# Kernel optimization log

Measured on AMD Instinct MI355X. Metric: run time of the kernel, lower is better.

## Reference

```python
import jax, jax.numpy as jnp
import numpy as np

DN = ('NCHW', 'OIHW', 'NCHW')

def conv1x1(x, w):
    return jax.lax.conv_general_dilated(x, w, (1, 1), 'VALID', dimension_numbers=DN)

def dwconv3(x, w):
    # depthwise 3x3, padding 1; w: (C,1,3,3)
    return jax.lax.conv_general_dilated(x, w, (1, 1), ((1, 1), (1, 1)),
                                        dimension_numbers=DN,
                                        feature_group_count=w.shape[0])

def ln_c(x, w, b, eps=1e-5):
    # Restormer-style LayerNorm over channel dim per spatial location (biased var)
    mu = x.mean(axis=1, keepdims=True)
    var = x.var(axis=1, keepdims=True)
    return (x - mu) / jnp.sqrt(var + eps) * w[None, :, None, None] + b[None, :, None, None]

def gelu(x):
    return jax.nn.gelu(x, approximate=False)

DIM = 128
NUM_HEADS = 2
B, H, W = 4, 192, 192
RED = 16

def setup_inputs() -> dict:
    key = jax.random.key(0)
    ks = jax.random.split(key, 20)
    s = 0.02
    d = DIM
    inp = {
        'x': jax.random.normal(ks[0], (B, d, H, W), jnp.float32),
        'ln_in_w': jnp.ones((d,), jnp.float32),
        'ln_in_b': jnp.zeros((d,), jnp.float32),
        'wq_pw': jax.random.normal(ks[1], (d, d, 1, 1), jnp.float32) * s,
        'wq_dw': jax.random.normal(ks[2], (d, 1, 3, 3), jnp.float32) * s,
        'wk_pw': jax.random.normal(ks[3], (d, d, 1, 1), jnp.float32) * s,
        'wk_dw': jax.random.normal(ks[4], (d, 1, 3, 3), jnp.float32) * s,
        'wv_pw': jax.random.normal(ks[5], (d, d, 1, 1), jnp.float32) * s,
        'wv_dw': jax.random.normal(ks[6], (d, 1, 3, 3), jnp.float32) * s,
        'scale': jnp.ones((NUM_HEADS, 1, 1), jnp.float32),
        'ln_out_w': jnp.ones((d,), jnp.float32),
        'ln_out_b': jnp.zeros((d,), jnp.float32),
        'f1_pw': jax.random.normal(ks[7], (d, d, 1, 1), jnp.float32) * s,
        'f1_dw': jax.random.normal(ks[8], (d, 1, 3, 3), jnp.float32) * s,
        'f2_pw': jax.random.normal(ks[9], (d, d, 1, 1), jnp.float32) * s,
        'f2_dw': jax.random.normal(ks[10], (d, 1, 3, 3), jnp.float32) * s,
        'f_out': jax.random.normal(ks[11], (d, 2 * d, 1, 1), jnp.float32) * s,
        'g_w1': jax.random.normal(ks[12], (d // RED, d), jnp.float32) * s,
        'g_b1': jnp.zeros((d // RED,), jnp.float32),
        'g_w2': jax.random.normal(ks[13], (d, d // RED), jnp.float32) * s,
        'g_b2': jnp.zeros((d,), jnp.float32),
    }
    return inp

def reference(x, ln_in_w, ln_in_b, wq_pw, wq_dw, wk_pw, wk_dw, wv_pw, wv_dw,
              scale, ln_out_w, ln_out_b, f1_pw, f1_dw, f2_pw, f2_dw, f_out,
              g_w1, g_b1, g_w2, g_b2):
    b, c, h, w = x.shape
    n = scale.shape[0]
    hd = c // n
    xn = ln_c(x, ln_in_w, ln_in_b)
    # conv QKV: pointwise then depthwise
    q = dwconv3(conv1x1(xn, wq_pw), wq_dw).reshape(b, n, hd, h * w)
    k = dwconv3(conv1x1(xn, wk_pw), wk_dw).reshape(b, n, hd, h * w)
    v = dwconv3(conv1x1(xn, wv_pw), wv_dw).reshape(b, n, hd, h * w)
    # L2 normalize over the (large) hw dim, torch F.normalize semantics
    q = q / jnp.maximum(jnp.linalg.norm(q, axis=-1, keepdims=True), 1e-12)
    k = k / jnp.maximum(jnp.linalg.norm(k, axis=-1, keepdims=True), 1e-12)
    attn = jnp.einsum('bnch,bndh->bncd', q, k) * scale[None]  # (b,n,hd,hd)
    attn_weight = attn.reshape(b, n * hd, hd)
    a = jax.nn.softmax(attn, axis=-1)
    out = jnp.einsum('bncd,bndh->bnch', a, v).reshape(b, c, h, w)
    out = ln_c(out, ln_out_w, ln_out_b)
    # PreNorm FFN: two branches (1x1 -> GELU -> dw3x3), cat, GELU, 1x1 out
    o1 = dwconv3(gelu(conv1x1(out, f1_pw)), f1_dw)
    o2 = dwconv3(gelu(conv1x1(out, f2_pw)), f2_dw)
    ffn = conv1x1(gelu(jnp.concatenate([o1, o2], axis=1)), f_out)
    # ChannelGate (avg + max pools -> shared MLP -> sigmoid)
    def mlp(p):
        return jax.nn.relu(p @ g_w1.T + g_b1) @ g_w2.T + g_b2
    avg_p = ffn.mean(axis=(2, 3))
    max_p = ffn.max(axis=(2, 3))
    spec_score = jax.nn.sigmoid(mlp(avg_p) + mlp(max_p))
    return (spec_score, attn_weight)
```

## Files before the change

kernel.cpp:

```cpp
#include <hip/hip_runtime.h>
#include <math.h>

#define HW    36864
#define IMG   192

#define OFF_RS_QKV   0
#define OFF_B_QKV    384
#define OFF_RS_FFN   768
#define OFF_B_FFN    1024
#define OFF_SSQ      1280
#define OFF_AVG      2304
#define OFF_MAXK     2816
#define OFF_A        3328
#define OFF_MU1      36096
#define OFF_RSTD1    183552
#define OFF_MU2      331008
#define OFF_RSTD2    478464
#define OFF_PART     625920
#define OFF_AQH      2723072
#define OFF_AQL      2747648
#define OFF_AFH      2772224
#define OFF_AFL      2788608
#define OFF_AOH      2804992
#define OFF_AOL      2821376
#define OFF_BUF1     2837760

typedef __attribute__((ext_vector_type(8))) short short8v;
typedef __attribute__((ext_vector_type(4))) float floatx4;

__device__ __forceinline__ unsigned f2key(float f){
  unsigned b = __float_as_uint(f);
  return (b & 0x80000000u) ? ~b : (b | 0x80000000u);
}
__device__ __forceinline__ float key2f(unsigned k){
  return __uint_as_float((k & 0x80000000u) ? (k & 0x7fffffffu) : ~k);
}
__device__ __forceinline__ float gelu_f(float v){
  return 0.5f*v*(1.0f + erff(v*0.70710678118654752f));
}
__device__ __forceinline__ unsigned short bf16rn(float v){
  unsigned u = __float_as_uint(v);
  return (unsigned short)((u + 0x7FFFu + ((u>>16)&1u)) >> 16);
}
__device__ __forceinline__ float bf2f(unsigned short h){
  return __uint_as_float(((unsigned)h)<<16);
}

__global__ __launch_bounds__(256) void k_init(float* ws){
  int t = blockIdx.x*256 + threadIdx.x;
  if (t < 2048) ws[OFF_SSQ + t] = 0.0f;
}

__global__ void k_prep(const float* wq, const float* wk, const float* wv,
                       const float* f1, const float* f2, const float* fo,
                       const float* liw, const float* lib,
                       const float* low, const float* lob, float* ws){
  int t = blockIdx.x*256 + threadIdx.x;
  if (t < 384){
    const float* W = (t < 128) ? wq : (t < 256) ? wk : wv;
    int r = t & 127;
    float rs = 0.f, bs = 0.f;
    for (int c = 0; c < 128; c++){ float w = W[r*128+c]; rs += w*liw[c]; bs += w*lib[c]; }
    ws[OFF_RS_QKV+t] = rs; ws[OFF_B_QKV+t] = bs;
  } else if (t < 640){
    int m = t - 384;
    const float* W = (m < 128) ? f1 : f2;
    int r = m & 127;
    float rs = 0.f, bs = 0.f;
    for (int c = 0; c < 128; c++){ float w = W[r*128+c]; rs += w*low[c]; bs += w*lob[c]; }
    ws[OFF_RS_FFN+m] = rs; ws[OFF_B_FFN+m] = bs;
  }
  int e = t - 640;
  if (e < 0) return;
  unsigned short* aqh = (unsigned short*)(ws + OFF_AQH);
  unsigned short* aql = (unsigned short*)(ws + OFF_AQL);
  unsigned short* afh = (unsigned short*)(ws + OFF_AFH);
  unsigned short* afl = (unsigned short*)(ws + OFF_AFL);
  unsigned short* aoh = (unsigned short*)(ws + OFF_AOH);
  unsigned short* aol = (unsigned short*)(ws + OFF_AOL);
  if (e < 49152){
    int m = e>>7, k = e&127;
    const float* W = (m < 128) ? wq : (m < 256) ? wk : wv;
    float v = W[(m&127)*128 + k]*liw[k];
    unsigned short h = bf16rn(v);
    aqh[e] = h; aql[e] = bf16rn(v - bf2f(h));
  } else if (e < 81920){
    int e2 = e - 49152;
    int m = e2>>7, k = e2&127;
    const float* W = (m < 128) ? f1 : f2;
    float v = W[(m&127)*128 + k]*low[k];
    unsigned short h = bf16rn(v);
    afh[e2] = h; afl[e2] = bf16rn(v - bf2f(h));
  } else if (e < 114688){
    int e2 = e - 81920;
    float v = fo[e2];
    unsigned short h = bf16rn(v);
    aoh[e2] = h; aol[e2] = bf16rn(v - bf2f(h));
  }
}

__global__ __launch_bounds__(256) void k_stats(const float* __restrict__ x, float* __restrict__ ws){
  int t = threadIdx.x, b = blockIdx.y;
  int p0 = blockIdx.x*1024 + t*4;
  const float* xp = x + (size_t)b*128*HW + p0;
  float s[4] = {}, q[4] = {};
  #pragma unroll 4
  for (int c = 0; c < 128; c++){
    float4 v = *(const float4*)(xp + (size_t)c*HW);
    float vv[4] = {v.x,v.y,v.z,v.w};
    #pragma unroll
    for (int j = 0; j < 4; j++){ s[j] += vv[j]; q[j] += vv[j]*vv[j]; }
  }
  float mu[4], rs[4];
  #pragma unroll
  for (int j = 0; j < 4; j++){
    mu[j] = s[j]*(1.f/128.f);
    rs[j] = rsqrtf(q[j]*(1.f/128.f) - mu[j]*mu[j] + 1e-5f);
  }
  size_t g = (size_t)b*HW + p0;
  *(float4*)&ws[OFF_MU1 + g]   = make_float4(mu[0],mu[1],mu[2],mu[3]);
  *(float4*)&ws[OFF_RSTD1 + g] = make_float4(rs[0],rs[1],rs[2],rs[3]);
}

template<bool GELU>
__global__ __launch_bounds__(512,4) void k_gemm_mfma(
    const float* __restrict__ src, int src_bstride,
    const unsigned short* __restrict__ Ahi, const unsigned short* __restrict__ Alo,
    const float* __restrict__ rowsum, const float* __restrict__ bias,
    const float* __restrict__ mu, const float* __restrict__ rstd,
    float* __restrict__ dst, int dst_coff)
{
  __shared__ unsigned short BsH[2][8192];
  __shared__ unsigned short BsL[2][8192];
  int t = threadIdx.x;
  int m0 = blockIdx.x*128, p0 = blockIdx.y*128, b = blockIdx.z;
  int px0 = (t&63)<<1, kb0 = t>>6;
  int lane = t&63, wv = t>>6;
  int wm = (wv&3)*32, wn = (wv>>2)*64;
  int colg = lane&15, kg = lane>>4;
  float2 rv[8];
  const float* sbase = src + ((size_t)b*src_bstride)*HW + p0 + px0;

  auto loadreg = [&](int h){
    const float* sp = sbase + ((size_t)(h*64 + kb0*8))*HW;
    #pragma unroll
    for (int e = 0; e < 8; e++) rv[e] = *(const float2*)(sp + (size_t)e*HW);
  };
  auto convstore = [&](int bi){
    #pragma unroll
    for (int j = 0; j < 2; j++){
      int p = px0 + j;
      short8v hv, lv;
      #pragma unroll
      for (int e = 0; e < 8; e++){
        float v = (j==0) ? rv[e].x : rv[e].y;
        unsigned short hh = bf16rn(v);
        hv[e] = (short)hh; lv[e] = (short)bf16rn(v - bf2f(hh));
      }
      int o = (p<<6) + ((kb0 ^ (p&7))<<3);
      *(short8v*)&BsH[bi][o] = hv;
      *(short8v*)&BsL[bi][o] = lv;
    }
  };

  floatx4 acc[2][4];
  #pragma unroll
  for (int i = 0; i < 2; i++)
    #pragma unroll
    for (int j = 0; j < 4; j++) acc[i][j] = (floatx4){0.f,0.f,0.f,0.f};

  auto mfmah = [&](int bi, int h){
    #pragma unroll
    for (int kt = 0; kt < 2; kt++){
      int kb = kt*32 + kg*8;
      short8v ah[2], al[2], bh[4], bl[4];
      #pragma unroll
      for (int f = 0; f < 2; f++){
        size_t arow = (size_t)(m0 + wm + f*16 + colg)*128 + h*64 + kb;
        ah[f] = *(const short8v*)(Ahi + arow);
        al[f] = *(const short8v*)(Alo + arow);
      }
      #pragma unroll
      for (int f = 0; f < 4; f++){
        int p = wn + f*16 + colg;
        int o = (p<<6) + ((((kb>>3) ^ (p&7)))<<3);
        bh[f] = *(const short8v*)&BsH[bi][o];
        bl[f] = *(const short8v*)&BsL[bi][o];
      }
      #pragma unroll
      for (int i = 0; i < 2; i++)
        #pragma unroll
        for (int j = 0; j < 4; j++){
          acc[i][j] = __builtin_amdgcn_mfma_f32_16x16x32_bf16(al[i], bh[j], acc[i][j], 0,0,0);
          acc[i][j] = __builtin_amdgcn_mfma_f32_16x16x32_bf16(ah[i], bl[j], acc[i][j], 0,0,0);
          acc[i][j] = __builtin_amdgcn_mfma_f32_16x16x32_bf16(ah[i], bh[j], acc[i][j], 0,0,0);
        }
    }
  };

  loadreg(0); convstore(0);
  __syncthreads();
  loadreg(1);
  mfmah(0, 0);
  convstore(1);
  __syncthreads();
  mfmah(1, 1);

  int rowg = kg*4;
  const float* mub = mu   + (size_t)b*HW + p0;
  const float* rsb = rstd + (size_t)b*HW + p0;
  #pragma unroll
  for (int j = 0; j < 4; j++){
    int pc = wn + j*16 + colg;
    float muv = mub[pc], rsv = rsb[pc];
    #pragma unroll
    for (int i = 0; i < 2; i++){
      int mbase = m0 + wm + i*16 + rowg;
      float4 rs4 = *(const float4*)&rowsum[mbase];
      float4 bi4 = *(const float4*)&bias[mbase];
      float rsa[4] = {rs4.x,rs4.y,rs4.z,rs4.w};
      float bia[4] = {bi4.x,bi4.y,bi4.z,bi4.w};
      #pragma unroll
      for (int e = 0; e < 4; e++){
        float v = rsv*(acc[i][j][e] - muv*rsa[e]) + bia[e];
        if (GELU) v = gelu_f(v);
        dst[((size_t)(b*384 + dst_coff + mbase + e))*HW + p0 + pc] = v;
      }
    }
  }
}

template<bool GELU, bool SSQ>
__global__ __launch_bounds__(256) void k_dw(const float* __restrict__ src,
                                            const float* __restrict__ wdw,
                                            float* __restrict__ dst,
                                            float* __restrict__ ssq, int ssq_off){
  __shared__ float rows[10][194];
  __shared__ float wred[4];
  int t = threadIdx.x;
  int band = blockIdx.x, c = blockIdx.y, b = blockIdx.z;
  const float* sp = src + ((size_t)(b*384 + c))*HW;
  float w[9];
  #pragma unroll
  for (int j = 0; j < 9; j++) w[j] = wdw[c*9 + j];
  int r0 = band*8;
  for (int e = t; e < 1920; e += 256){
    int r = e/192, cc = e - r*192;
    int gr = r0 + r - 1;
    rows[r][cc+1] = (gr >= 0 && gr < IMG) ? sp[gr*IMG + cc] : 0.f;
  }
  if (t < 20) rows[t>>1][(t&1)*193] = 0.f;
  __syncthreads();
  float s2 = 0.f;
  float* dp = dst + ((size_t)(b*384 + c))*HW + r0*IMG;
  #pragma unroll
  for (int i = 0; i < 6; i++){
    int px = i*256 + t;
    int r = px/192, cc = px - r*192;
    float v = 0.f;
    #pragma unroll
    for (int dy = 0; dy < 3; dy++)
      #pragma unroll
      for (int dx = 0; dx < 3; dx++)
        v += rows[r+dy][cc+dx] * w[dy*3+dx];
    if (GELU) v = gelu_f(v);
    dp[px] = v;
    if (SSQ) s2 += v*v;
  }
  if (SSQ){
    #pragma unroll
    for (int off = 32; off; off >>= 1) s2 += __shfl_xor(s2, off);
    if ((t & 63) == 0) wred[t>>6] = s2;
    __syncthreads();
    if (t == 0) atomicAdd(&ssq[b*256 + ssq_off + c], wred[0]+wred[1]+wred[2]+wred[3]);
  }
}

__global__ __launch_bounds__(256,4) void k_qk(const float* __restrict__ buf,
                                              float* __restrict__ part){
  __shared__ float qs[64][68];
  __shared__ float ks[64][68];
  int t = threadIdx.x;
  int chunk = blockIdx.x, h = blockIdx.y, b = blockIdx.z;
  int tc = (t>>4)<<2, td = (t&15)<<2;
  int c = t>>2, pq = (t&3)<<4;
  const float* qp = buf + ((size_t)(b*384 + 256 + h*64 + c))*HW + chunk*576 + pq;
  const float* kp = buf + ((size_t)(b*384 +       h*64 + c))*HW + chunk*576 + pq;
  float acc[4][4] = {};
  for (int st = 0; st < 9; st++){
    __syncthreads();
    #pragma unroll
    for (int u = 0; u < 4; u++){
      float4 qv = *(const float4*)(qp + st*64 + u*4);
      float4 kv = *(const float4*)(kp + st*64 + u*4);
      int p = pq + u*4;
      qs[p+0][c] = qv.x; qs[p+1][c] = qv.y; qs[p+2][c] = qv.z; qs[p+3][c] = qv.w;
      ks[p+0][c] = kv.x; ks[p+1][c] = kv.y; ks[p+2][c] = kv.z; ks[p+3][c] = kv.w;
    }
    __syncthreads();
    #pragma unroll 4
    for (int p = 0; p < 64; p++){
      float4 q4 = *(const float4*)&qs[p][tc];
      float4 k4 = *(const float4*)&ks[p][td];
      float qa[4] = {q4.x,q4.y,q4.z,q4.w};
      float ka[4] = {k4.x,k4.y,k4.z,k4.w};
      #pragma unroll
      for (int i = 0; i < 4; i++)
        #pragma unroll
        for (int j = 0; j < 4; j++) acc[i][j] += qa[i]*ka[j];
    }
  }
  float* pp = part + ((size_t)((b*2+h)*64 + chunk))*4096;
  #pragma unroll
  for (int i = 0; i < 4; i++)
    *(float4*)&pp[(tc+i)*64 + td] = make_float4(acc[i][0],acc[i][1],acc[i][2],acc[i][3]);
}

__global__ __launch_bounds__(256) void k_softmax(const float* __restrict__ part,
                                                 const float* __restrict__ ssq,
                                                 const float* __restrict__ scale,
                                                 float* __restrict__ ws_a,
                                                 float* __restrict__ out)
{
  __shared__ float red[8][64];
  __shared__ float rnk[64];
  int t = threadIdx.x;
  int c0 = blockIdx.x*8, h = blockIdx.y, b = blockIdx.z;
  int bh = b*2 + h;
  const float* pp = part + (size_t)bh*64*4096;
  for (int e = t; e < 512; e += 256){
    int c = e>>6, d = e&63;
    float s = 0.f;
    for (int ch = 0; ch < 64; ch++) s += pp[(size_t)ch*4096 + (c0+c)*64 + d];
    red[c][d] = s;
  }
  if (t < 64) rnk[t] = 1.0f/fmaxf(sqrtf(ssq[b*256 + 128 + h*64 + t]), 1e-12f);
  __syncthreads();
  if (t < 8){
    int c = c0 + t;
    float rq = (1.0f/fmaxf(sqrtf(ssq[b*256 + h*64 + c]), 1e-12f))*scale[h];
    float vals[64], vmax = -1e30f;
    for (int d = 0; d < 64; d++){
      float v = red[t][d]*rq*rnk[d];
      vals[d] = v; vmax = fmaxf(vmax, v);
    }
    float* aw = out + 512 + ((size_t)(b*128 + h*64 + c))*64;
    for (int d = 0; d < 64; d++) aw[d] = vals[d];
    float se = 0.f;
    for (int d = 0; d < 64; d++){ float e = expf(vals[d]-vmax); vals[d] = e; se += e; }
    float inv = 1.0f/se;
    float* ar = ws_a + ((size_t)(b*128 + h*64 + c))*64;
    for (int d = 0; d < 64; d++) ar[d] = vals[d]*inv;
  }
}

__global__ __launch_bounds__(256,2) void k_av(const float* __restrict__ ws_a,
                                              const float* __restrict__ buf,
                                              float* __restrict__ dst,
                                              float* __restrict__ mu2,
                                              float* __restrict__ rstd2)
{
  __shared__ float a_t[64][128];
  __shared__ float v_l[128][64];
  int t = threadIdx.x;
  int pt = blockIdx.x, b = blockIdx.y;
  int p0 = pt*64;
  {
    int c = t>>1, dh = (t&1)<<5;
    const float* ap = ws_a + ((size_t)(b*128 + c))*64 + dh;
    #pragma unroll
    for (int u = 0; u < 8; u++){
      float4 v = *(const float4*)(ap + u*4);
      int d = dh + u*4;
      a_t[d+0][c] = v.x; a_t[d+1][c] = v.y; a_t[d+2][c] = v.z; a_t[d+3][c] = v.w;
    }
    const float* vp = buf + ((size_t)(b*384 + 256 + c))*HW + p0 + dh;
    #pragma unroll
    for (int u = 0; u < 8; u++)
      *(float4*)&v_l[c][dh + u*4] = *(const float4*)(vp + u*4);
  }
  __syncthreads();
  int tm = (t>>4)<<3, tp = (t&15)<<2;
  int hd = tm>>6;
  float acc[8][4] = {};
  #pragma unroll 2
  for (int d = 0; d < 64; d++){
    float4 v4 = *(const float4*)&v_l[hd*64+d][tp];
    float vv[4] = {v4.x,v4.y,v4.z,v4.w};
    #pragma unroll
    for (int i = 0; i < 8; i++){
      float av = a_t[d][tm+i];
      #pragma unroll
      for (int j = 0; j < 4; j++) acc[i][j] += av*vv[j];
    }
  }
  #pragma unroll
  for (int i = 0; i < 8; i++)
    *(float4*)(dst + ((size_t)(b*384 + tm+i))*HW + p0 + tp)
        = make_float4(acc[i][0],acc[i][1],acc[i][2],acc[i][3]);
  __syncthreads();
  float* px = &a_t[0][0];
  if (t < 128) px[t] = 0.f;
  __syncthreads();
  #pragma unroll
  for (int j = 0; j < 4; j++){
    float s = 0.f, q = 0.f;
    #pragma unroll
    for (int i = 0; i < 8; i++){ s += acc[i][j]; q += acc[i][j]*acc[i][j]; }
    atomicAdd(&px[tp+j], s);
    atomicAdd(&px[64+tp+j], q);
  }
  __syncthreads();
  if (t < 64){
    float mu  = px[t]*(1.f/128.f);
    float var = px[64+t]*(1.f/128.f) - mu*mu;
    mu2[(size_t)b*HW + p0 + t]   = mu;
    rstd2[(size_t)b*HW + p0 + t] = rsqrtf(var + 1e-5f);
  }
}

__global__ __launch_bounds__(512,4) void k_fout_mfma(
    const float* __restrict__ bufz,
    const unsigned short* __restrict__ Ahi, const unsigned short* __restrict__ Alo,
    float* __restrict__ avg, unsigned* __restrict__ maxk)
{
  __shared__ unsigned short BsH[2][8192];
  __shared__ unsigned short BsL[2][8192];
  __shared__ float osum[128];
  __shared__ unsigned okey[128];
  int t = threadIdx.x;
  int p0 = blockIdx.x*128, b = blockIdx.y;
  if (t < 128){ osum[t] = 0.f; okey[t] = 0u; }
  int px0 = (t&63)<<1, kb0 = t>>6;
  int lane = t&63, wv = t>>6;
  int wm = (wv&3)*32, wn = (wv>>2)*64;
  int colg = lane&15, kg = lane>>4;
  float2 rv[8];
  const float* sbase = bufz + ((size_t)b*384)*HW + p0 + px0;

  auto loadreg = [&](int h){
    const float* sp = sbase + ((size_t)(h*64 + kb0*8))*HW;
    #pragma unroll
    for (int e = 0; e < 8; e++) rv[e] = *(const float2*)(sp + (size_t)e*HW);
  };
  auto convstore = [&](int bi){
    #pragma unroll
    for (int j = 0; j < 2; j++){
      int p = px0 + j;
      short8v hv, lv;
      #pragma unroll
      for (int e = 0; e < 8; e++){
        float v = (j==0) ? rv[e].x : rv[e].y;
        unsigned short hh = bf16rn(v);
        hv[e] = (short)hh; lv[e] = (short)bf16rn(v - bf2f(hh));
      }
      int o = (p<<6) + ((kb0 ^ (p&7))<<3);
      *(short8v*)&BsH[bi][o] = hv;
      *(short8v*)&BsL[bi][o] = lv;
    }
  };

  floatx4 acc[2][4];
  #pragma unroll
  for (int i = 0; i < 2; i++)
    #pragma unroll
    for (int j = 0; j < 4; j++) acc[i][j] = (floatx4){0.f,0.f,0.f,0.f};

  auto mfmah = [&](int bi, int h){
    #pragma unroll
    for (int kt = 0; kt < 2; kt++){
      int kb = kt*32 + kg*8;
      short8v ah[2], al[2], bh[4], bl[4];
      #pragma unroll
      for (int f = 0; f < 2; f++){
        size_t arow = (size_t)(wm + f*16 + colg)*256 + h*64 + kb;
        ah[f] = *(const short8v*)(Ahi + arow);
        al[f] = *(const short8v*)(Alo + arow);
      }
      #pragma unroll
      for (int f = 0; f < 4; f++){
        int p = wn + f*16 + colg;
        int o = (p<<6) + ((((kb>>3) ^ (p&7)))<<3);
        bh[f] = *(const short8v*)&BsH[bi][o];
        bl[f] = *(const short8v*)&BsL[bi][o];
      }
      #pragma unroll
      for (int i = 0; i < 2; i++)
        #pragma unroll
        for (int j = 0; j < 4; j++){
          acc[i][j] = __builtin_amdgcn_mfma_f32_16x16x32_bf16(al[i], bh[j], acc[i][j], 0,0,0);
          acc[i][j] = __builtin_amdgcn_mfma_f32_16x16x32_bf16(ah[i], bl[j], acc[i][j], 0,0,0);
          acc[i][j] = __builtin_amdgcn_mfma_f32_16x16x32_bf16(ah[i], bh[j], acc[i][j], 0,0,0);
        }
    }
  };

  loadreg(0); convstore(0);
  __syncthreads();
  #pragma unroll
  for (int h = 1; h < 4; h++){
    loadreg(h);
    mfmah((h-1)&1, h-1);
    convstore(h&1);
    __syncthreads();
  }
  mfmah(1, 3);

  int rowg = kg*4;
  #pragma unroll
  for (int i = 0; i < 2; i++){
    #pragma unroll
    for (int e = 0; e < 4; e++){
      float s = 0.f, mx = -1e30f;
      #pragma unroll
      for (int j = 0; j < 4; j++){ float v = acc[i][j][e]; s += v; mx = fmaxf(mx, v); }
      #pragma unroll
      for (int off = 1; off < 16; off <<= 1){
        s += __shfl_xor(s, off);
        mx = fmaxf(mx, __shfl_xor(mx, off));
      }
      if (colg == 0){
        int oc = wm + i*16 + rowg + e;
        atomicAdd(&osum[oc], s);
        atomicMax(&okey[oc], f2key(mx));
      }
    }
  }
  __syncthreads();
  if (t < 128){
    atomicAdd(&avg[b*128+t], osum[t]);
    atomicMax(&maxk[b*128+t], okey[t]);
  }
}

__global__ __launch_bounds__(128) void k_gate(const float* __restrict__ avg,
                                              const unsigned* __restrict__ maxk,
                                              const float* __restrict__ w1, const float* __restrict__ b1,
                                              const float* __restrict__ w2, const float* __restrict__ b2,
                                              float* __restrict__ out)
{
  __shared__ float ap[128], mp[128], h1a[8], h1m[8];
  int t = threadIdx.x, b = blockIdx.x;
  ap[t] = avg[b*128+t]*(1.0f/36864.0f);
  mp[t] = key2f(maxk[b*128+t]);
  __syncthreads();
  if (t < 8){
    float sa = b1[t], sm = b1[t];
    for (int c = 0; c < 128; c++){ float w = w1[t*128+c]; sa += w*ap[c]; sm += w*mp[c]; }
    h1a[t] = fmaxf(sa, 0.f); h1m[t] = fmaxf(sm, 0.f);
  }
  __syncthreads();
  float y = 2.0f*b2[t];
  for (int r = 0; r < 8; r++) y += w2[t*8+r]*(h1a[r]+h1m[r]);
  out[b*128+t] = 1.0f/(1.0f+expf(-y));
}

extern "C" void kernel_launch(void* const* d_in, const int* in_sizes, int n_in,
                              void* d_out, int out_size, void* d_ws, size_t ws_size,
                              hipStream_t stream)
{
  const float* x        = (const float*)d_in[0];
  const float* ln_in_w  = (const float*)d_in[1];
  const float* ln_in_b  = (const float*)d_in[2];
  const float* wq_pw    = (const float*)d_in[3];
  const float* wq_dw    = (const float*)d_in[4];
  const float* wk_pw    = (const float*)d_in[5];
  const float* wk_dw    = (const float*)d_in[6];
  const float* wv_pw    = (const float*)d_in[7];
  const float* wv_dw    = (const float*)d_in[8];
  const float* scale    = (const float*)d_in[9];
  const float* ln_out_w = (const float*)d_in[10];
  const float* ln_out_b = (const float*)d_in[11];
  const float* f1_pw    = (const float*)d_in[12];
  const float* f1_dw    = (const float*)d_in[13];
  const float* f2_pw    = (const float*)d_in[14];
  const float* f2_dw    = (const float*)d_in[15];
  const float* f_out    = (const float*)d_in[16];
  const float* g_w1     = (const float*)d_in[17];
  const float* g_b1     = (const float*)d_in[18];
  const float* g_w2     = (const float*)d_in[19];
  const float* g_b2     = (const float*)d_in[20];
  float* ws  = (float*)d_ws;
  float* out = (float*)d_out;
  float* BUF = ws + OFF_BUF1;
  const unsigned short* aqh = (const unsigned short*)(ws + OFF_AQH);
  const unsigned short* aql = (const unsigned short*)(ws + OFF_AQL);
  const unsigned short* afh = (const unsigned short*)(ws + OFF_AFH);
  const unsigned short* afl = (const unsigned short*)(ws + OFF_AFL);
  const unsigned short* aoh = (const unsigned short*)(ws + OFF_AOH);
  const unsigned short* aol = (const unsigned short*)(ws + OFF_AOL);

  k_init<<<dim3(8), dim3(256), 0, stream>>>(ws);
  k_prep<<<dim3(451), dim3(256), 0, stream>>>(wq_pw, wk_pw, wv_pw, f1_pw, f2_pw, f_out,
                                              ln_in_w, ln_in_b, ln_out_w, ln_out_b, ws);
  k_stats<<<dim3(36,4), dim3(256), 0, stream>>>(x, ws);
  k_gemm_mfma<false><<<dim3(2,288,4), dim3(512), 0, stream>>>(
      x, 128, aqh, aql, ws+OFF_RS_QKV, ws+OFF_B_QKV,
      ws+OFF_MU1, ws+OFF_RSTD1, BUF, 0);
  k_dw<false,true><<<dim3(24,128,4), dim3(256), 0, stream>>>(
      BUF, wq_dw, BUF + (size_t)256*HW, ws+OFF_SSQ, 0);
  k_dw<false,true><<<dim3(24,128,4), dim3(256), 0, stream>>>(
      BUF + (size_t)128*HW, wk_dw, BUF, ws+OFF_SSQ, 128);
  k_qk<<<dim3(64,2,4), dim3(256), 0, stream>>>(BUF, ws+OFF_PART);
  k_softmax<<<dim3(8,2,4), dim3(256), 0, stream>>>(
      ws+OFF_PART, ws+OFF_SSQ, scale, ws+OFF_A, out);
  k_gemm_mfma<false><<<dim3(1,288,4), dim3(512), 0, stream>>>(
      x, 128, aqh + 256*128, aql + 256*128, ws+OFF_RS_QKV+256, ws+OFF_B_QKV+256,
      ws+OFF_MU1, ws+OFF_RSTD1, BUF, 128);
  k_dw<false,false><<<dim3(24,128,4), dim3(256), 0, stream>>>(
      BUF + (size_t)128*HW, wv_dw, BUF + (size_t)256*HW, nullptr, 0);
  k_av<<<dim3(576,4), dim3(256), 0, stream>>>(
      ws+OFF_A, BUF, BUF, ws+OFF_MU2, ws+OFF_RSTD2);
  k_gemm_mfma<true><<<dim3(2,288,4), dim3(512), 0, stream>>>(
      BUF, 384, afh, afl, ws+OFF_RS_FFN, ws+OFF_B_FFN,
      ws+OFF_MU2, ws+OFF_RSTD2, BUF, 128);
  k_dw<true,false><<<dim3(24,128,4), dim3(256), 0, stream>>>(
      BUF + (size_t)128*HW, f1_dw, BUF, nullptr, 0);
  k_dw<true,false><<<dim3(24,128,4), dim3(256), 0, stream>>>(
      BUF + (size_t)256*HW, f2_dw, BUF + (size_t)128*HW, nullptr, 0);
  k_fout_mfma<<<dim3(288,4), dim3(512), 0, stream>>>(
      BUF, aoh, aol, ws+OFF_AVG, (unsigned*)(ws+OFF_MAXK));
  k_gate<<<dim3(4), dim3(128), 0, stream>>>(
      ws+OFF_AVG, (const unsigned*)(ws+OFF_MAXK), g_w1, g_b1, g_w2, g_b2, out);

  (void)in_sizes; (void)n_in; (void)out_size; (void)ws_size;
}
```

Baseline: 755.6 us.

## Store intermediates as bf16 and drop low-part MFMA term on activations

```diff
diff --git a/kernel.cpp b/kernel.cpp
--- a/kernel.cpp
+++ b/kernel.cpp
@@ -23,9 +23,11 @@
 #define OFF_AFL      2788608
 #define OFF_AOH      2804992
 #define OFF_AOL      2821376
-#define OFF_BUF1     2837760
+#define OFF_BUFA     2837760
+#define OFF_BUFB     31149312
 
 typedef __attribute__((ext_vector_type(8))) short short8v;
+typedef __attribute__((ext_vector_type(4))) unsigned short ushort4v;
 typedef __attribute__((ext_vector_type(4))) float floatx4;
 
 __device__ __forceinline__ unsigned f2key(float f){
@@ -44,6 +46,9 @@
 }
 __device__ __forceinline__ float bf2f(unsigned short h){
   return __uint_as_float(((unsigned)h)<<16);
+}
+__device__ __forceinline__ int bofs(int p, int k8){
+  return (p<<6) + ((k8 ^ (p&7) ^ ((p>>3)&7))<<3);
 }
 
 __global__ __launch_bounds__(256) void k_init(float* ws){
@@ -122,16 +127,15 @@
   *(float4*)&ws[OFF_RSTD1 + g] = make_float4(rs[0],rs[1],rs[2],rs[3]);
 }
 
-template<bool GELU>
-__global__ __launch_bounds__(512,4) void k_gemm_mfma(
-    const float* __restrict__ src, int src_bstride,
+template<bool GELU, bool SRCBF16>
+__global__ __launch_bounds__(512,8) void k_gemm_mfma(
+    const void* __restrict__ srcv, int src_bstride,
     const unsigned short* __restrict__ Ahi, const unsigned short* __restrict__ Alo,
     const float* __restrict__ rowsum, const float* __restrict__ bias,
     const float* __restrict__ mu, const float* __restrict__ rstd,
-    float* __restrict__ dst, int dst_coff)
+    unsigned short* __restrict__ dst, int dst_coff)
 {
-  __shared__ unsigned short BsH[2][8192];
-  __shared__ unsigned short BsL[2][8192];
+  __shared__ unsigned short Bs[2][8192];
   int t = threadIdx.x;
   int m0 = blockIdx.x*128, p0 = blockIdx.y*128, b = blockIdx.z;
   int px0 = (t&63)<<1, kb0 = t>>6;
@@ -139,27 +143,35 @@
   int wm = (wv&3)*32, wn = (wv>>2)*64;
   int colg = lane&15, kg = lane>>4;
   float2 rv[8];
-  const float* sbase = src + ((size_t)b*src_bstride)*HW + p0 + px0;
+  unsigned rv16[8];
+  const float* sbase32 = SRCBF16 ? (const float*)nullptr
+      : ((const float*)srcv + ((size_t)b*src_bstride)*HW + p0 + px0);
+  const unsigned short* sbase16 = SRCBF16
+      ? ((const unsigned short*)srcv + ((size_t)b*src_bstride)*HW + p0 + px0)
+      : (const unsigned short*)nullptr;
 
   auto loadreg = [&](int h){
-    const float* sp = sbase + ((size_t)(h*64 + kb0*8))*HW;
-    #pragma unroll
-    for (int e = 0; e < 8; e++) rv[e] = *(const float2*)(sp + (size_t)e*HW);
+    if (SRCBF16){
+      const unsigned short* sp = sbase16 + ((size_t)(h*64 + kb0*8))*HW;
+      #pragma unroll
+      for (int e = 0; e < 8; e++) rv16[e] = *(const unsigned*)(sp + (size_t)e*HW);
+    } else {
+      const float* sp = sbase32 + ((size_t)(h*64 + kb0*8))*HW;
+      #pragma unroll
+      for (int e = 0; e < 8; e++) rv[e] = *(const float2*)(sp + (size_t)e*HW);
+    }
   };
   auto convstore = [&](int bi){
     #pragma unroll
     for (int j = 0; j < 2; j++){
       int p = px0 + j;
-      short8v hv, lv;
+      short8v hv;
       #pragma unroll
       for (int e = 0; e < 8; e++){
-        float v = (j==0) ? rv[e].x : rv[e].y;
-        unsigned short hh = bf16rn(v);
-        hv[e] = (short)hh; lv[e] = (short)bf16rn(v - bf2f(hh));
+        if (SRCBF16) hv[e] = (short)(unsigned short)((j==0) ? (rv16[e]&0xFFFFu) : (rv16[e]>>16));
+        else         hv[e] = (short)bf16rn((j==0)?rv[e].x:rv[e].y);
       }
-      int o = (p<<6) + ((kb0 ^ (p&7))<<3);
-      *(short8v*)&BsH[bi][o] = hv;
-      *(short8v*)&BsL[bi][o] = lv;
+      *(short8v*)&Bs[bi][bofs(p, kb0)] = hv;
     }
   };
 
@@ -173,7 +185,7 @@
     #pragma unroll
     for (int kt = 0; kt < 2; kt++){
       int kb = kt*32 + kg*8;
-      short8v ah[2], al[2], bh[4], bl[4];
+      short8v ah[2], al[2], bh[4];
       #pragma unroll
       for (int f = 0; f < 2; f++){
         size_t arow = (size_t)(m0 + wm + f*16 + colg)*128 + h*64 + kb;
@@ -181,18 +193,13 @@
         al[f] = *(const short8v*)(Alo + arow);
       }
       #pragma unroll
-      for (int f = 0; f < 4; f++){
-        int p = wn + f*16 + colg;
-        int o = (p<<6) + ((((kb>>3) ^ (p&7)))<<3);
-        bh[f] = *(const short8v*)&BsH[bi][o];
-        bl[f] = *(const short8v*)&BsL[bi][o];
-      }
+      for (int f = 0; f < 4; f++)
+        bh[f] = *(const short8v*)&Bs[bi][bofs(wn + f*16 + colg, kb>>3)];
       #pragma unroll
       for (int i = 0; i < 2; i++)
         #pragma unroll
         for (int j = 0; j < 4; j++){
           acc[i][j] = __builtin_amdgcn_mfma_f32_16x16x32_bf16(al[i], bh[j], acc[i][j], 0,0,0);
-          acc[i][j] = __builtin_amdgcn_mfma_f32_16x16x32_bf16(ah[i], bl[j], acc[i][j], 0,0,0);
           acc[i][j] = __builtin_amdgcn_mfma_f32_16x16x32_bf16(ah[i], bh[j], acc[i][j], 0,0,0);
         }
     }
@@ -224,48 +231,57 @@
       for (int e = 0; e < 4; e++){
         float v = rsv*(acc[i][j][e] - muv*rsa[e]) + bia[e];
         if (GELU) v = gelu_f(v);
-        dst[((size_t)(b*384 + dst_coff + mbase + e))*HW + p0 + pc] = v;
+        dst[((size_t)(b*384 + dst_coff + mbase + e))*HW + p0 + pc] = bf16rn(v);
       }
     }
   }
 }
 
 template<bool GELU, bool SSQ>
-__global__ __launch_bounds__(256) void k_dw(const float* __restrict__ src,
+__global__ __launch_bounds__(256) void k_dw(const unsigned short* __restrict__ src,
                                             const float* __restrict__ wdw,
-                                            float* __restrict__ dst,
+                                            unsigned short* __restrict__ dst,
                                             float* __restrict__ ssq, int ssq_off){
   __shared__ float rows[10][194];
   __shared__ float wred[4];
   int t = threadIdx.x;
   int band = blockIdx.x, c = blockIdx.y, b = blockIdx.z;
-  const float* sp = src + ((size_t)(b*384 + c))*HW;
+  const unsigned short* sp = src + ((size_t)(b*384 + c))*HW;
   float w[9];
   #pragma unroll
   for (int j = 0; j < 9; j++) w[j] = wdw[c*9 + j];
   int r0 = band*8;
-  for (int e = t; e < 1920; e += 256){
-    int r = e/192, cc = e - r*192;
+  for (int e = t; e < 960; e += 256){
+    int r = e/96, c2 = e - r*96;
     int gr = r0 + r - 1;
-    rows[r][cc+1] = (gr >= 0 && gr < IMG) ? sp[gr*IMG + cc] : 0.f;
+    unsigned pv = (gr >= 0 && gr < IMG) ? *(const unsigned*)(sp + gr*IMG + c2*2) : 0u;
+    rows[r][c2*2+1] = bf2f((unsigned short)(pv & 0xFFFFu));
+    rows[r][c2*2+2] = bf2f((unsigned short)(pv >> 16));
   }
   if (t < 20) rows[t>>1][(t&1)*193] = 0.f;
   __syncthreads();
   float s2 = 0.f;
-  float* dp = dst + ((size_t)(b*384 + c))*HW + r0*IMG;
-  #pragma unroll
-  for (int i = 0; i < 6; i++){
-    int px = i*256 + t;
-    int r = px/192, cc = px - r*192;
-    float v = 0.f;
+  unsigned short* dp = dst + ((size_t)(b*384 + c))*HW + r0*IMG;
+  #pragma unroll
+  for (int i = 0; i < 3; i++){
+    int pi = i*256 + t;
+    int r = pi/96, cp = pi - r*96;
+    float v0 = 0.f, v1 = 0.f;
     #pragma unroll
     for (int dy = 0; dy < 3; dy++)
       #pragma unroll
-      for (int dx = 0; dx < 3; dx++)
-        v += rows[r+dy][cc+dx] * w[dy*3+dx];
-    if (GELU) v = gelu_f(v);
-    dp[px] = v;
-    if (SSQ) s2 += v*v;
+      for (int dx = 0; dx < 3; dx++){
+        float wv = w[dy*3+dx];
+        v0 += rows[r+dy][cp*2+dx]   * wv;
+        v1 += rows[r+dy][cp*2+1+dx] * wv;
+      }
+    if (GELU){ v0 = gelu_f(v0); v1 = gelu_f(v1); }
+    unsigned short u0 = bf16rn(v0), u1 = bf16rn(v1);
+    if (SSQ){
+      float f0 = bf2f(u0), f1 = bf2f(u1);
+      s2 += f0*f0 + f1*f1;
+    }
+    *(unsigned*)(dp + r*IMG + cp*2) = (unsigned)u0 | ((unsigned)u1 << 16);
   }
   if (SSQ){
     #pragma unroll
@@ -276,7 +292,7 @@
   }
 }
 
-__global__ __launch_bounds__(256,4) void k_qk(const float* __restrict__ buf,
+__global__ __launch_bounds__(256,4) void k_qk(const unsigned short* __restrict__ buf,
                                               float* __restrict__ part){
   __shared__ float qs[64][68];
   __shared__ float ks[64][68];
@@ -284,18 +300,21 @@
   int chunk = blockIdx.x, h = blockIdx.y, b = blockIdx.z;
   int tc = (t>>4)<<2, td = (t&15)<<2;
   int c = t>>2, pq = (t&3)<<4;
-  const float* qp = buf + ((size_t)(b*384 + 256 + h*64 + c))*HW + chunk*576 + pq;
-  const float* kp = buf + ((size_t)(b*384 +       h*64 + c))*HW + chunk*576 + pq;
+  const unsigned short* qp = buf + ((size_t)(b*384 +       h*64 + c))*HW + chunk*576 + pq;
+  const unsigned short* kp = buf + ((size_t)(b*384 + 128 + h*64 + c))*HW + chunk*576 + pq;
   float acc[4][4] = {};
   for (int st = 0; st < 9; st++){
     __syncthreads();
-    #pragma unroll
-    for (int u = 0; u < 4; u++){
-      float4 qv = *(const float4*)(qp + st*64 + u*4);
-      float4 kv = *(const float4*)(kp + st*64 + u*4);
-      int p = pq + u*4;
-      qs[p+0][c] = qv.x; qs[p+1][c] = qv.y; qs[p+2][c] = qv.z; qs[p+3][c] = qv.w;
-      ks[p+0][c] = kv.x; ks[p+1][c] = kv.y; ks[p+2][c] = kv.z; ks[p+3][c] = kv.w;
+    short8v q0 = *(const short8v*)(qp + st*64);
+    short8v q1 = *(const short8v*)(qp + st*64 + 8);
+    short8v k0 = *(const short8v*)(kp + st*64);
+    short8v k1 = *(const short8v*)(kp + st*64 + 8);
+    #pragma unroll
+    for (int u = 0; u < 8; u++){
+      qs[pq+u][c]   = bf2f((unsigned short)q0[u]);
+      qs[pq+8+u][c] = bf2f((unsigned short)q1[u]);
+      ks[pq+u][c]   = bf2f((unsigned short)k0[u]);
+      ks[pq+8+u][c] = bf2f((unsigned short)k1[u]);
     }
     __syncthreads();
     #pragma unroll 4
@@ -355,8 +374,8 @@
 }
 
 __global__ __launch_bounds__(256,2) void k_av(const float* __restrict__ ws_a,
-                                              const float* __restrict__ buf,
-                                              float* __restrict__ dst,
+                                              const unsigned short* __restrict__ buf,
+                                              unsigned short* __restrict__ dst,
                                               float* __restrict__ mu2,
                                               float* __restrict__ rstd2)
 {
@@ -374,10 +393,13 @@
       int d = dh + u*4;
       a_t[d+0][c] = v.x; a_t[d+1][c] = v.y; a_t[d+2][c] = v.z; a_t[d+3][c] = v.w;
     }
-    const float* vp = buf + ((size_t)(b*384 + 256 + c))*HW + p0 + dh;
-    #pragma unroll
-    for (int u = 0; u < 8; u++)
-      *(float4*)&v_l[c][dh + u*4] = *(const float4*)(vp + u*4);
+    const unsigned short* vp = buf + ((size_t)(b*384 + 256 + c))*HW + p0 + dh;
+    #pragma unroll
+    for (int u = 0; u < 4; u++){
+      short8v v8 = *(const short8v*)(vp + u*8);
+      #pragma unroll
+      for (int z = 0; z < 8; z++) v_l[c][dh + u*8 + z] = bf2f((unsigned short)v8[z]);
+    }
   }
   __syncthreads();
   int tm = (t>>4)<<3, tp = (t&15)<<2;
@@ -395,9 +417,16 @@
     }
   }
   #pragma unroll
-  for (int i = 0; i < 8; i++)
-    *(float4*)(dst + ((size_t)(b*384 + tm+i))*HW + p0 + tp)
-        = make_float4(acc[i][0],acc[i][1],acc[i][2],acc[i][3]);
+  for (int i = 0; i < 8; i++){
+    ushort4v u4;
+    #pragma unroll
+    for (int j = 0; j < 4; j++){
+      unsigned short us = bf16rn(acc[i][j]);
+      acc[i][j] = bf2f(us);
+      u4[j] = us;
+    }
+    *(ushort4v*)(dst + ((size_t)(b*384 + tm+i))*HW + p0 + tp) = u4;
+  }
   __syncthreads();
   float* px = &a_t[0][0];
   if (t < 128) px[t] = 0.f;
@@ -419,13 +448,12 @@
   }
 }
 
-__global__ __launch_bounds__(512,4) void k_fout_mfma(
-    const float* __restrict__ bufz,
+__global__ __launch_bounds__(512,8) void k_fout_mfma(
+    const unsigned short* __restrict__ bufz,
     const unsigned short* __restrict__ Ahi, const unsigned short* __restrict__ Alo,
     float* __restrict__ avg, unsigned* __restrict__ maxk)
 {
-  __shared__ unsigned short BsH[2][8192];
-  __shared__ unsigned short BsL[2][8192];
+  __shared__ unsigned short Bs[2][8192];
   __shared__ float osum[128];
   __shared__ unsigned okey[128];
   int t = threadIdx.x;
@@ -435,28 +463,23 @@
   int lane = t&63, wv = t>>6;
   int wm = (wv&3)*32, wn = (wv>>2)*64;
   int colg = lane&15, kg = lane>>4;
-  float2 rv[8];
-  const float* sbase = bufz + ((size_t)b*384)*HW + p0 + px0;
+  unsigned rv16[8];
+  const unsigned short* sbase = bufz + ((size_t)b*384)*HW + p0 + px0;
 
   auto loadreg = [&](int h){
-    const float* sp = sbase + ((size_t)(h*64 + kb0*8))*HW;
-    #pragma unroll
-    for (int e = 0; e < 8; e++) rv[e] = *(const float2*)(sp + (size_t)e*HW);
+    const unsigned short* sp = sbase + ((size_t)(h*64 + kb0*8))*HW;
+    #pragma unroll
+    for (int e = 0; e < 8; e++) rv16[e] = *(const unsigned*)(sp + (size_t)e*HW);
   };
   auto convstore = [&](int bi){
     #pragma unroll
     for (int j = 0; j < 2; j++){
       int p = px0 + j;
-      short8v hv, lv;
-      #pragma unroll
-      for (int e = 0; e < 8; e++){
-        float v = (j==0) ? rv[e].x : rv[e].y;
-        unsigned short hh = bf16rn(v);
-        hv[e] = (short)hh; lv[e] = (short)bf16rn(v - bf2f(hh));
-      }
-      int o = (p<<6) + ((kb0 ^ (p&7))<<3);
-      *(short8v*)&BsH[bi][o] = hv;
-      *(short8v*)&BsL[bi][o] = lv;
+      short8v hv;
+      #pragma unroll
+      for (int e = 0; e < 8; e++)
+        hv[e] = (short)(unsigned short)((j==0) ? (rv16[e]&0xFFFFu) : (rv16[e]>>16));
+      *(short8v*)&Bs[bi][bofs(p, kb0)] = hv;
     }
   };
 
@@ -470,7 +493,7 @@
     #pragma unroll
     for (int kt = 0; kt < 2; kt++){
       int kb = kt*32 + kg*8;
-      short8v ah[2], al[2], bh[4], bl[4];
+      short8v ah[2], al[2], bh[4];
       #pragma unroll
       for (int f = 0; f < 2; f++){
         size_t arow = (size_t)(wm + f*16 + colg)*256 + h*64 + kb;
@@ -478,18 +501,13 @@
         al[f] = *(const short8v*)(Alo + arow);
       }
       #pragma unroll
-      for (int f = 0; f < 4; f++){
-        int p = wn + f*16 + colg;
-        int o = (p<<6) + ((((kb>>3) ^ (p&7)))<<3);
-        bh[f] = *(const short8v*)&BsH[bi][o];
-        bl[f] = *(const short8v*)&BsL[bi][o];
-      }
+      for (int f = 0; f < 4; f++)
+        bh[f] = *(const short8v*)&Bs[bi][bofs(wn + f*16 + colg, kb>>3)];
       #pragma unroll
       for (int i = 0; i < 2; i++)
         #pragma unroll
         for (int j = 0; j < 4; j++){
           acc[i][j] = __builtin_amdgcn_mfma_f32_16x16x32_bf16(al[i], bh[j], acc[i][j], 0,0,0);
-          acc[i][j] = __builtin_amdgcn_mfma_f32_16x16x32_bf16(ah[i], bl[j], acc[i][j], 0,0,0);
           acc[i][j] = __builtin_amdgcn_mfma_f32_16x16x32_bf16(ah[i], bh[j], acc[i][j], 0,0,0);
         }
     }
@@ -582,7 +600,8 @@
   const float* g_b2     = (const float*)d_in[20];
   float* ws  = (float*)d_ws;
   float* out = (float*)d_out;
-  float* BUF = ws + OFF_BUF1;
+  unsigned short* BUFA = (unsigned short*)(ws + OFF_BUFA);
+  unsigned short* BUFB = (unsigned short*)(ws + OFF_BUFB);
   const unsigned short* aqh = (const unsigned short*)(ws + OFF_AQH);
   const unsigned short* aql = (const unsigned short*)(ws + OFF_AQL);
   const unsigned short* afh = (const unsigned short*)(ws + OFF_AFH);
@@ -594,32 +613,29 @@
   k_prep<<<dim3(451), dim3(256), 0, stream>>>(wq_pw, wk_pw, wv_pw, f1_pw, f2_pw, f_out,
                                               ln_in_w, ln_in_b, ln_out_w, ln_out_b, ws);
   k_stats<<<dim3(36,4), dim3(256), 0, stream>>>(x, ws);
-  k_gemm_mfma<false><<<dim3(2,288,4), dim3(512), 0, stream>>>(
+  k_gemm_mfma<false,false><<<dim3(3,288,4), dim3(512), 0, stream>>>(
       x, 128, aqh, aql, ws+OFF_RS_QKV, ws+OFF_B_QKV,
-      ws+OFF_MU1, ws+OFF_RSTD1, BUF, 0);
+      ws+OFF_MU1, ws+OFF_RSTD1, BUFA, 0);
   k_dw<false,true><<<dim3(24,128,4), dim3(256), 0, stream>>>(
-      BUF, wq_dw, BUF + (size_t)256*HW, ws+OFF_SSQ, 0);
+      BUFA, wq_dw, BUFB, ws+OFF_SSQ, 0);
   k_dw<false,true><<<dim3(24,128,4), dim3(256), 0, stream>>>(
-      BUF + (size_t)128*HW, wk_dw, BUF, ws+OFF_SSQ, 128);
-  k_qk<<<dim3(64,2,4), dim3(256), 0, stream>>>(BUF, ws+OFF_PART);
+      BUFA + (size_t)128*HW, wk_dw, BUFB + (size_t)128*HW, ws+OFF_SSQ, 128);
+  k_dw<false,false><<<dim3(24,128,4), dim3(256), 0, stream>>>(
+      BUFA + (size_t)256*HW, wv_dw, BUFB + (size_t)256*HW, nullptr, 0);
+  k_qk<<<dim3(64,2,4), dim3(256), 0, stream>>>(BUFB, ws+OFF_PART);
   k_softmax<<<dim3(8,2,4), dim3(256), 0, stream>>>(
       ws+OFF_PART, ws+OFF_SSQ, scale, ws+OFF_A, out);
-  k_gemm_mfma<false><<<dim3(1,288,4), dim3(512), 0, stream>>>(
-      x, 128, aqh + 256*128, aql + 256*128, ws+OFF_RS_QKV+256, ws+OFF_B_QKV+256,
-      ws+OFF_MU1, ws+OFF_RSTD1, BUF, 128);
-  k_dw<false,false><<<dim3(24,128,4), dim3(256), 0, stream>>>(
-      BUF + (size_t)128*HW, wv_dw, BUF + (size_t)256*HW, nullptr, 0);
   k_av<<<dim3(576,4), dim3(256), 0, stream>>>(
-      ws+OFF_A, BUF, BUF, ws+OFF_MU2, ws+OFF_RSTD2);
-  k_gemm_mfma<true><<<dim3(2,288,4), dim3(512), 0, stream>>>(
-      BUF, 384, afh, afl, ws+OFF_RS_FFN, ws+OFF_B_FFN,
-      ws+OFF_MU2, ws+OFF_RSTD2, BUF, 128);
+      ws+OFF_A, BUFB, BUFA, ws+OFF_MU2, ws+OFF_RSTD2);
+  k_gemm_mfma<true,true><<<dim3(2,288,4), dim3(512), 0, stream>>>(
+      BUFA, 384, afh, afl, ws+OFF_RS_FFN, ws+OFF_B_FFN,
+      ws+OFF_MU2, ws+OFF_RSTD2, BUFA, 128);
   k_dw<true,false><<<dim3(24,128,4), dim3(256), 0, stream>>>(
-      BUF + (size_t)128*HW, f1_dw, BUF, nullptr, 0);
+      BUFA + (size_t)128*HW, f1_dw, BUFB, nullptr, 0);
   k_dw<true,false><<<dim3(24,128,4), dim3(256), 0, stream>>>(
-      BUF + (size_t)256*HW, f2_dw, BUF + (size_t)128*HW, nullptr, 0);
+      BUFA + (size_t)256*HW, f2_dw, BUFB + (size_t)128*HW, nullptr, 0);
   k_fout_mfma<<<dim3(288,4), dim3(512), 0, stream>>>(
-      BUF, aoh, aol, ws+OFF_AVG, (unsigned*)(ws+OFF_MAXK));
+      BUFB, aoh, aol, ws+OFF_AVG, (unsigned*)(ws+OFF_MAXK));
   k_gate<<<dim3(4), dim3(128), 0, stream>>>(
       ws+OFF_AVG, (const unsigned*)(ws+OFF_MAXK), g_w1, g_b1, g_w2, g_b2, out);
 
```

After: 845.3 us. +11.9%, slower.
